# Performance work log

Hardware: AMD Instinct MI355X
Metric: run time of the kernel (lower is better)

The kernel has to match this reference:

```python
import jax, jax.numpy as jnp
import numpy as np

N = 50000      # num nodes
E = 600000     # num edges
D = 128        # num_node_features (in == out)
R = 8          # num_relations


def setup_inputs() -> dict:
    key = jax.random.key(0)
    k = jax.random.split(key, 6)
    x = jax.random.normal(k[0], (N, D), dtype=jnp.float32)
    edge_index = jax.random.randint(k[1], (2, E), 0, N, dtype=jnp.int32)
    edge_type = jax.random.randint(k[2], (E,), 0, R, dtype=jnp.int32)
    scale = 1.0 / np.sqrt(D).astype(np.float32)
    weight = jax.random.normal(k[3], (R, D, D), dtype=jnp.float32) * scale  # per-relation W_r
    root = jax.random.normal(k[4], (D, D), dtype=jnp.float32) * scale       # self-loop weight
    bias = jnp.zeros((D,), dtype=jnp.float32)
    return {"x": x, "edge_index": edge_index, "edge_type": edge_type,
            "weight": weight, "root": root, "bias": bias}


def _rgcn(x, weight, root, bias, edge_index, edge_type):
    # RGCNConv (PyG defaults: aggr='mean' per relation, root weight + bias)
    src, dst = edge_index[0], edge_index[1]
    # combined segment id over (relation, dst) so one segment_sum covers all relations
    seg = edge_type * N + dst                              # [E]
    msgs = x[src]                                          # [E, D] gather
    sums = jax.ops.segment_sum(msgs, seg, num_segments=R * N)                 # [R*N, D]
    cnts = jax.ops.segment_sum(jnp.ones((E, 1), x.dtype), seg, num_segments=R * N)
    mean = sums / jnp.maximum(cnts, 1.0)                   # mean over neighbors, 0 if none
    agg = mean.reshape(R, N, D)
    out = jnp.einsum('rnd,rde->ne', agg, weight) + x @ root + bias
    return out


def reference(x, edge_index, edge_type, weight, root, bias):
    return jax.nn.relu(_rgcn(x, weight, root, bias, edge_index, edge_type))
```

## Files before the change

kernel.cpp:

```cpp
#include <hip/hip_runtime.h>

constexpr int NN = 50000;
constexpr int NE = 600000;
constexpr int D  = 128;
constexpr int NR = 8;
constexpr int KT = (NR + 1) * D;
constexpr int NSEG = NN * NR;

constexpr int SCAN_ELEMS = 1024;
constexpr int NBLK2 = (NSEG + SCAN_ELEMS - 1) / SCAN_ELEMS;

typedef unsigned int   u32;
typedef unsigned short u16;
typedef float  f32x4 __attribute__((ext_vector_type(4)));
typedef short  s16x8 __attribute__((ext_vector_type(8)));

__device__ __forceinline__ u16 f2bf(float f) {
    u32 u = __float_as_uint(f);
    u32 r = (u + 0x7fffu + ((u >> 16) & 1u)) >> 16;
    return (u16)r;
}

__device__ __forceinline__ void async_cp16(const void* g, void* l) {
    __builtin_amdgcn_global_load_lds(
        (const __attribute__((address_space(1))) u32*)g,
        (__attribute__((address_space(3))) u32*)l, 16, 0, 0);
}

__global__ __launch_bounds__(256) void prep_all(const float* __restrict__ x,
                                                const float* __restrict__ weight,
                                                const float* __restrict__ root,
                                                const int* __restrict__ dst,
                                                const int* __restrict__ et,
                                                u16* __restrict__ xb,
                                                u16* __restrict__ wt9,
                                                int* __restrict__ cnt2) {
    const int NX4 = NN * D / 4;
    const int NW  = (NR + 1) * D * D;
    int gid = blockIdx.x * 256 + threadIdx.x;
    if (gid < NX4) {
        int i = gid * 4;
        float4 v = *(const float4*)(x + i);
        ushort4 o;
        o.x = f2bf(v.x); o.y = f2bf(v.y); o.z = f2bf(v.z); o.w = f2bf(v.w);
        *(ushort4*)(xb + i) = o;
        return;
    }
    int g = gid - NX4;
    if (g < NW) {
        int p = g >> 14;
        int idx = g & 16383;
        int n = idx >> 7, k = idx & 127;
        float v = (p == 0) ? root[k * D + n]
                           : weight[(size_t)(p - 1) * D * D + k * D + n];
        wt9[(size_t)p * 16384 + idx] = f2bf(v);
        return;
    }
    int e = g - NW;
    if (e < NE) atomicAdd(&cnt2[dst[e] * NR + et[e]], 1);
}

__global__ __launch_bounds__(256) void scan1(const int* __restrict__ cnt,
                                             int* __restrict__ offs,
                                             int* __restrict__ bsums) {
    __shared__ int lds[256];
    int t = threadIdx.x;
    int base = blockIdx.x * SCAN_ELEMS + t * 4;
    int v0 = (base + 0 < NSEG) ? cnt[base + 0] : 0;
    int v1 = (base + 1 < NSEG) ? cnt[base + 1] : 0;
    int v2 = (base + 2 < NSEG) ? cnt[base + 2] : 0;
    int v3 = (base + 3 < NSEG) ? cnt[base + 3] : 0;
    int s = v0 + v1 + v2 + v3;
    lds[t] = s;
    __syncthreads();
    int val = s;
    for (int off = 1; off < 256; off <<= 1) {
        int tmp = (t >= off) ? lds[t - off] : 0;
        __syncthreads();
        val += tmp;
        lds[t] = val;
        __syncthreads();
    }
    int ex = val - s;
    if (base + 0 < NSEG) offs[base + 0] = ex;
    if (base + 1 < NSEG) offs[base + 1] = ex + v0;
    if (base + 2 < NSEG) offs[base + 2] = ex + v0 + v1;
    if (base + 3 < NSEG) offs[base + 3] = ex + v0 + v1 + v2;
    if (t == 255) bsums[blockIdx.x] = val;
}

__global__ __launch_bounds__(512) void scan2(int* __restrict__ bsums) {
    __shared__ int lds[512];
    int t = threadIdx.x;
    int v = (t < NBLK2) ? bsums[t] : 0;
    lds[t] = v;
    __syncthreads();
    int val = v;
    for (int off = 1; off < 512; off <<= 1) {
        int tmp = (t >= off) ? lds[t - off] : 0;
        __syncthreads();
        val += tmp;
        lds[t] = val;
        __syncthreads();
    }
    if (t < NBLK2) bsums[t] = val - v;
}

__global__ __launch_bounds__(256) void scan3(int* __restrict__ offs,
                                             int* __restrict__ cur,
                                             const int* __restrict__ bsums) {
    int i = blockIdx.x * 256 + threadIdx.x;
    if (i < NSEG) {
        int v = offs[i] + bsums[i >> 10];
        offs[i] = v;
        cur[i]  = v;
    }
    if (i == 0) offs[NSEG] = NE;
}

__global__ __launch_bounds__(256) void fill_bins(const int* __restrict__ src,
                                                 const int* __restrict__ dst,
                                                 const int* __restrict__ et,
                                                 int* __restrict__ cur,
                                                 int* __restrict__ ebin) {
    int e = blockIdx.x * 256 + threadIdx.x;
    if (e >= NE) return;
    int r = et[e];
    int idx = atomicAdd(&cur[dst[e] * NR + r], 1);
    ebin[idx] = (r << 16) | src[e];
}

__global__ __launch_bounds__(128) void aggregate_kernel(const u32* __restrict__ xw,
                                                        const int* __restrict__ offs2,
                                                        const int* __restrict__ ebin,
                                                        u32* __restrict__ sw) {
    const int lane = threadIdx.x & 63;
    const int n = blockIdx.x * 2 + (threadIdx.x >> 6);
    if (n >= NN) return;
    const int beg = __builtin_amdgcn_readfirstlane(offs2[n * NR]);
    const int c   = __builtin_amdgcn_readfirstlane(offs2[n * NR + NR]) - beg;

    float a0 = 0.f, a1 = 0.f;
    int r_cur = 0, cnt_cur = 0;

    int q0 = 0, q1 = 0, q2 = 0, q3 = 0, q4 = 0, q5 = 0, q6 = 0, q7 = 0;
    u32 v0 = 0, v1 = 0, v2 = 0, v3 = 0, v4 = 0, v5 = 0, v6 = 0, v7 = 0;

#define REFILL(Q, V, IDX)                                                   \
    if ((IDX) < c) {                                                        \
        Q = __builtin_amdgcn_readfirstlane(ebin[beg + (IDX)]);              \
        V = xw[(size_t)((u32)Q & 0xffffu) * 64 + lane];                     \
    }
#define FLUSH()                                                             \
    {                                                                       \
        float inv_ = 1.0f / (float)(cnt_cur > 0 ? cnt_cur : 1);             \
        u32 lo16_ = f2bf(a0 * inv_);                                        \
        u32 hi16_ = f2bf(a1 * inv_);                                        \
        sw[((size_t)r_cur * NN + n) * 64 + lane] = lo16_ | (hi16_ << 16);   \
        a0 = 0.f; a1 = 0.f; cnt_cur = 0; ++r_cur;                           \
    }
#define CONSUME(Q, V)                                                       \
    {                                                                       \
        int rj_ = (int)((u32)(Q) >> 16);                                    \
        while (r_cur < rj_) FLUSH()                                         \
        a0 += __uint_as_float((V) << 16);                                   \
        a1 += __uint_as_float((V) & 0xffff0000u);                           \
        ++cnt_cur;                                                          \
    }

    REFILL(q0, v0, 0) REFILL(q1, v1, 1) REFILL(q2, v2, 2) REFILL(q3, v3, 3)
    REFILL(q4, v4, 4) REFILL(q5, v5, 5) REFILL(q6, v6, 6) REFILL(q7, v7, 7)

    int e = 0;
    for (; e + 8 <= c; e += 8) {
        CONSUME(q0, v0) REFILL(q0, v0, e + 8)
        CONSUME(q1, v1) REFILL(q1, v1, e + 9)
        CONSUME(q2, v2) REFILL(q2, v2, e + 10)
        CONSUME(q3, v3) REFILL(q3, v3, e + 11)
        CONSUME(q4, v4) REFILL(q4, v4, e + 12)
        CONSUME(q5, v5) REFILL(q5, v5, e + 13)
        CONSUME(q6, v6) REFILL(q6, v6, e + 14)
        CONSUME(q7, v7) REFILL(q7, v7, e + 15)
    }
    if (e + 0 < c) CONSUME(q0, v0)
    if (e + 1 < c) CONSUME(q1, v1)
    if (e + 2 < c) CONSUME(q2, v2)
    if (e + 3 < c) CONSUME(q3, v3)
    if (e + 4 < c) CONSUME(q4, v4)
    if (e + 5 < c) CONSUME(q5, v5)
    if (e + 6 < c) CONSUME(q6, v6)
    if (e + 7 < c) CONSUME(q7, v7)

    while (r_cur < NR) FLUSH()
#undef REFILL
#undef FLUSH
#undef CONSUME
}

__global__ __launch_bounds__(256) void mfma_gemm(const u16* __restrict__ xb,
                                                 const u16* __restrict__ sums,
                                                 const u16* __restrict__ wt9,
                                                 const float* __restrict__ bias,
                                                 float* __restrict__ out) {
    __shared__ __align__(16) u16 Bs[2][128 * 64];

    const int tid  = threadIdx.x;
    const int wave = tid >> 6;
    const int lane = tid & 63;
    const int m0   = blockIdx.x * 64;
    const int fr   = lane & 15;
    const int l4   = lane >> 4;
    const int fk   = l4 * 8;

    int boff[4];
#pragma unroll
    for (int r = 0; r < 4; ++r) {
        int p = r * 256 + tid;
        int g = p ^ ((p >> 3) & 7);
        boff[r] = (g >> 3) * D + (g & 7) * 8;
    }
    int bidx[16];
#pragma unroll
    for (int h = 0; h < 2; ++h)
#pragma unroll
        for (int nt = 0; nt < 8; ++nt) {
            int gl = (nt * 16 + fr) * 8 + h * 4 + l4;
            int pp = gl ^ ((gl >> 3) & 7);
            bidx[h * 8 + nt] = pp * 8;
        }

    int r0 = m0 + wave * 16 + fr;  if (r0 > NN - 1) r0 = NN - 1;
    const size_t aoff = (size_t)r0 * D + fk;

    auto stage = [&](u16* bufp, const u16* Bp) {
#pragma unroll
        for (int r = 0; r < 4; ++r)
            async_cp16(Bp + boff[r], (char*)bufp + (size_t)(r * 256 + tid) * 16);
    };

    f32x4 acc[8];
#pragma unroll
    for (int j = 0; j < 8; ++j) acc[j] = (f32x4){0.f, 0.f, 0.f, 0.f};

    stage(&Bs[0][0], wt9);
    s16x8 a0c = *(const s16x8*)(xb + aoff);
    s16x8 a1c = *(const s16x8*)(xb + aoff + 32);
    __builtin_amdgcn_sched_barrier(0);

    for (int it = 0; it < 17; ++it) {
        const int nx  = it + 1;
        const int npl = nx >> 1;
        const int kof = (nx & 1) * 64;
        u16* nbuf = &Bs[nx & 1][0];
        const u16* cbuf = &Bs[it & 1][0];

        stage(nbuf, wt9 + npl * 16384 + kof);
        const u16* Ap = ((npl == 0) ? xb : sums + (size_t)(npl - 1) * NN * D) + kof;
        s16x8 a0n = *(const s16x8*)(Ap + aoff);
        s16x8 a1n = *(const s16x8*)(Ap + aoff + 32);
        __builtin_amdgcn_sched_barrier(0);
        asm volatile("s_waitcnt vmcnt(6)" ::: "memory");
        __builtin_amdgcn_s_barrier();
        __builtin_amdgcn_sched_barrier(0);
#pragma unroll
        for (int nt = 0; nt < 8; ++nt) {
            s16x8 bf = *(const s16x8*)(cbuf + bidx[nt]);
            acc[nt] = __builtin_amdgcn_mfma_f32_16x16x32_bf16(a0c, bf, acc[nt], 0, 0, 0);
        }
#pragma unroll
        for (int nt = 0; nt < 8; ++nt) {
            s16x8 bf = *(const s16x8*)(cbuf + bidx[8 + nt]);
            acc[nt] = __builtin_amdgcn_mfma_f32_16x16x32_bf16(a1c, bf, acc[nt], 0, 0, 0);
        }
        asm volatile("s_waitcnt lgkmcnt(0)" ::: "memory");
        __builtin_amdgcn_sched_barrier(0);
        __builtin_amdgcn_s_barrier();
        __builtin_amdgcn_sched_barrier(0);
        a0c = a0n; a1c = a1n;
    }
    asm volatile("s_waitcnt vmcnt(0)" ::: "memory");
    __builtin_amdgcn_s_barrier();
    __builtin_amdgcn_sched_barrier(0);
    {
        const u16* cbuf = &Bs[1][0];
#pragma unroll
        for (int nt = 0; nt < 8; ++nt) {
            s16x8 bf = *(const s16x8*)(cbuf + bidx[nt]);
            acc[nt] = __builtin_amdgcn_mfma_f32_16x16x32_bf16(a0c, bf, acc[nt], 0, 0, 0);
        }
#pragma unroll
        for (int nt = 0; nt < 8; ++nt) {
            s16x8 bf = *(const s16x8*)(cbuf + bidx[8 + nt]);
            acc[nt] = __builtin_amdgcn_mfma_f32_16x16x32_bf16(a1c, bf, acc[nt], 0, 0, 0);
        }
    }

    const int cl = lane & 15;
    const int rq = l4 * 4;
#pragma unroll
    for (int nt = 0; nt < 8; ++nt) {
        int col = nt * 16 + cl;
        float bv = bias[col];
#pragma unroll
        for (int reg = 0; reg < 4; ++reg) {
            int n = m0 + wave * 16 + rq + reg;
            if (n < NN) {
                float v = acc[nt][reg] + bv;
                out[(size_t)n * D + col] = fmaxf(v, 0.0f);
            }
        }
    }
}

extern "C" void kernel_launch(void* const* d_in, const int* in_sizes, int n_in,
                              void* d_out, int out_size, void* d_ws, size_t ws_size,
                              hipStream_t stream) {
    const float* x      = (const float*)d_in[0];
    const int*   ei     = (const int*)d_in[1];
    const int*   et     = (const int*)d_in[2];
    const float* weight = (const float*)d_in[3];
    const float* root   = (const float*)d_in[4];
    const float* bias   = (const float*)d_in[5];
    float* out = (float*)d_out;
    const int* srcv = ei;
    const int* dstv = ei + NE;

    int* cnt2  = (int*)d_ws;
    int* cur2  = cnt2 + NSEG;
    int* offs2 = cur2 + NSEG;
    int* bsums = offs2 + NSEG + 1;
    int* ebin  = bsums + 512;
    size_t fixed_b  = ((char*)(ebin + NE) - (char*)d_ws);
    size_t fixed_al = (fixed_b + 255) & ~(size_t)255;
    u16* xb   = (u16*)((char*)d_ws + fixed_al);
    u16* sums = xb + (size_t)NN * D;
    u16* wt9  = sums + (size_t)NR * NN * D;

    hipMemsetAsync(cnt2, 0, NSEG * sizeof(int), stream);

    const int PREP = NN * D / 4 + (NR + 1) * D * D + NE;
    prep_all<<<(PREP + 255) / 256, 256, 0, stream>>>(x, weight, root, dstv, et,
                                                     xb, wt9, cnt2);

    scan1<<<NBLK2, 256, 0, stream>>>(cnt2, offs2, bsums);
    scan2<<<1, 512, 0, stream>>>(bsums);
    scan3<<<(NSEG + 256) / 256, 256, 0, stream>>>(offs2, cur2, bsums);
    fill_bins<<<(NE + 255) / 256, 256, 0, stream>>>(srcv, dstv, et, cur2, ebin);

    aggregate_kernel<<<(NN + 1) / 2, 128, 0, stream>>>((const u32*)xb, offs2, ebin,
                                                       (u32*)sums);

    mfma_gemm<<<(NN + 63) / 64, 256, 0, stream>>>(xb, sums, wt9, bias, out);
}
```

Baseline: 219.3 us.

## Fuse neighbor aggregation into MFMA GEMM via per-wave LDS scratch

Segments are re-keyed relation-major (rel*N+dst) so each wave can gather the neighbor means for its 16 rows one relation at a time. The means go into a swizzled LDS scratch and feed the MFMA A operand directly, removing the separate aggregate kernel and the 8xNxD bf16 sums buffer round-trip through global memory. The cost is that gather latency now sits inside the GEMM block's schedule. The gather also runs serially per relation with barriers between stages, which may reduce overlap and occupancy because of the extra LDS.

```diff
diff --git a/kernel.cpp b/kernel.cpp
--- a/kernel.cpp
+++ b/kernel.cpp
@@ -4,7 +4,6 @@
 constexpr int NE = 600000;
 constexpr int D  = 128;
 constexpr int NR = 8;
-constexpr int KT = (NR + 1) * D;
 constexpr int NSEG = NN * NR;
 
 constexpr int SCAN_ELEMS = 1024;
@@ -57,7 +56,7 @@
         return;
     }
     int e = g - NW;
-    if (e < NE) atomicAdd(&cnt2[dst[e] * NR + et[e]], 1);
+    if (e < NE) atomicAdd(&cnt2[et[e] * NN + dst[e]], 1);
 }
 
 __global__ __launch_bounds__(256) void scan1(const int* __restrict__ cnt,
@@ -125,92 +124,29 @@
                                                  int* __restrict__ ebin) {
     int e = blockIdx.x * 256 + threadIdx.x;
     if (e >= NE) return;
-    int r = et[e];
-    int idx = atomicAdd(&cur[dst[e] * NR + r], 1);
-    ebin[idx] = (r << 16) | src[e];
-}
-
-__global__ __launch_bounds__(128) void aggregate_kernel(const u32* __restrict__ xw,
-                                                        const int* __restrict__ offs2,
-                                                        const int* __restrict__ ebin,
-                                                        u32* __restrict__ sw) {
-    const int lane = threadIdx.x & 63;
-    const int n = blockIdx.x * 2 + (threadIdx.x >> 6);
-    if (n >= NN) return;
-    const int beg = __builtin_amdgcn_readfirstlane(offs2[n * NR]);
-    const int c   = __builtin_amdgcn_readfirstlane(offs2[n * NR + NR]) - beg;
-
-    float a0 = 0.f, a1 = 0.f;
-    int r_cur = 0, cnt_cur = 0;
-
-    int q0 = 0, q1 = 0, q2 = 0, q3 = 0, q4 = 0, q5 = 0, q6 = 0, q7 = 0;
-    u32 v0 = 0, v1 = 0, v2 = 0, v3 = 0, v4 = 0, v5 = 0, v6 = 0, v7 = 0;
-
-#define REFILL(Q, V, IDX)                                                   \
-    if ((IDX) < c) {                                                        \
-        Q = __builtin_amdgcn_readfirstlane(ebin[beg + (IDX)]);              \
-        V = xw[(size_t)((u32)Q & 0xffffu) * 64 + lane];                     \
-    }
-#define FLUSH()                                                             \
-    {                                                                       \
-        float inv_ = 1.0f / (float)(cnt_cur > 0 ? cnt_cur : 1);             \
-        u32 lo16_ = f2bf(a0 * inv_);                                        \
-        u32 hi16_ = f2bf(a1 * inv_);                                        \
-        sw[((size_t)r_cur * NN + n) * 64 + lane] = lo16_ | (hi16_ << 16);   \
-        a0 = 0.f; a1 = 0.f; cnt_cur = 0; ++r_cur;                           \
-    }
-#define CONSUME(Q, V)                                                       \
-    {                                                                       \
-        int rj_ = (int)((u32)(Q) >> 16);                                    \
-        while (r_cur < rj_) FLUSH()                                         \
-        a0 += __uint_as_float((V) << 16);                                   \
-        a1 += __uint_as_float((V) & 0xffff0000u);                           \
-        ++cnt_cur;                                                          \
-    }
-
-    REFILL(q0, v0, 0) REFILL(q1, v1, 1) REFILL(q2, v2, 2) REFILL(q3, v3, 3)
-    REFILL(q4, v4, 4) REFILL(q5, v5, 5) REFILL(q6, v6, 6) REFILL(q7, v7, 7)
-
-    int e = 0;
-    for (; e + 8 <= c; e += 8) {
-        CONSUME(q0, v0) REFILL(q0, v0, e + 8)
-        CONSUME(q1, v1) REFILL(q1, v1, e + 9)
-        CONSUME(q2, v2) REFILL(q2, v2, e + 10)
-        CONSUME(q3, v3) REFILL(q3, v3, e + 11)
-        CONSUME(q4, v4) REFILL(q4, v4, e + 12)
-        CONSUME(q5, v5) REFILL(q5, v5, e + 13)
-        CONSUME(q6, v6) REFILL(q6, v6, e + 14)
-        CONSUME(q7, v7) REFILL(q7, v7, e + 15)
-    }
-    if (e + 0 < c) CONSUME(q0, v0)
-    if (e + 1 < c) CONSUME(q1, v1)
-    if (e + 2 < c) CONSUME(q2, v2)
-    if (e + 3 < c) CONSUME(q3, v3)
-    if (e + 4 < c) CONSUME(q4, v4)
-    if (e + 5 < c) CONSUME(q5, v5)
-    if (e + 6 < c) CONSUME(q6, v6)
-    if (e + 7 < c) CONSUME(q7, v7)
-
-    while (r_cur < NR) FLUSH()
-#undef REFILL
-#undef FLUSH
-#undef CONSUME
-}
-
-__global__ __launch_bounds__(256) void mfma_gemm(const u16* __restrict__ xb,
-                                                 const u16* __restrict__ sums,
-                                                 const u16* __restrict__ wt9,
-                                                 const float* __restrict__ bias,
-                                                 float* __restrict__ out) {
+    int d = dst[e];
+    int idx = atomicAdd(&cur[et[e] * NN + d], 1);
+    ebin[idx] = (d << 16) | src[e];
+}
+
+__global__ __launch_bounds__(256) void rgcn_fused(const u16* __restrict__ xb,
+                                                  const u16* __restrict__ wt9,
+                                                  const int* __restrict__ offs2,
+                                                  const int* __restrict__ ebin,
+                                                  const float* __restrict__ bias,
+                                                  float* __restrict__ out) {
     __shared__ __align__(16) u16 Bs[2][128 * 64];
+    __shared__ __align__(16) u16 Sc[4][2048];
 
     const int tid  = threadIdx.x;
     const int wave = tid >> 6;
     const int lane = tid & 63;
     const int m0   = blockIdx.x * 64;
+    const int n0   = m0 + wave * 16;
     const int fr   = lane & 15;
     const int l4   = lane >> 4;
-    const int fk   = l4 * 8;
+    const u32* xw  = (const u32*)xb;
+    u16* scratch   = &Sc[wave][0];
 
     int boff[4];
 #pragma unroll
@@ -229,8 +165,10 @@
             bidx[h * 8 + nt] = pp * 8;
         }
 
-    int r0 = m0 + wave * 16 + fr;  if (r0 > NN - 1) r0 = NN - 1;
-    const size_t aoff = (size_t)r0 * D + fk;
+    int sro[4];
+#pragma unroll
+    for (int ks = 0; ks < 4; ++ks)
+        sro[ks] = fr * 128 + (((ks * 4 + l4) ^ (fr & 7)) * 8);
 
     auto stage = [&](u16* bufp, const u16* Bp) {
 #pragma unroll
@@ -238,62 +176,139 @@
             async_cp16(Bp + boff[r], (char*)bufp + (size_t)(r * 256 + tid) * 16);
     };
 
+    auto gather = [&](int rel) {
+        int nlo  = n0 < NN ? n0 : NN;
+        int nhi2 = (n0 + 16) < NN ? (n0 + 16) : NN;
+        int gbeg = __builtin_amdgcn_readfirstlane(offs2[rel * NN + nlo]);
+        int gc   = __builtin_amdgcn_readfirstlane(offs2[rel * NN + nhi2]) - gbeg;
+        float a0 = 0.f, a1 = 0.f;
+        int cur = 0, cnt_cur = 0;
+        int q0 = 0, q1 = 0, q2 = 0, q3 = 0, q4 = 0, q5 = 0, q6 = 0, q7 = 0;
+        u32 w0 = 0, w1 = 0, w2 = 0, w3 = 0, w4 = 0, w5 = 0, w6 = 0, w7 = 0;
+#define GREFILL(Q, V, IDX)                                                  \
+        if ((IDX) < gc) {                                                   \
+            Q = __builtin_amdgcn_readfirstlane(ebin[gbeg + (IDX)]);         \
+            V = xw[(size_t)((u32)Q & 0xffffu) * 64 + lane];                 \
+        }
+#define GFLUSH()                                                            \
+        {                                                                   \
+            float inv_ = 1.0f / (float)(cnt_cur > 0 ? cnt_cur : 1);         \
+            u32 lo_ = f2bf(a0 * inv_);                                      \
+            u32 hi_ = f2bf(a1 * inv_);                                      \
+            *(u32*)(scratch + cur * 128 + (((lane >> 2) ^ (cur & 7)) << 3)  \
+                    + ((2 * lane) & 7)) = lo_ | (hi_ << 16);                \
+            a0 = 0.f; a1 = 0.f; cnt_cur = 0; ++cur;                         \
+        }
+#define GCONSUME(Q, V)                                                      \
+        {                                                                   \
+            int nd_ = (int)((u32)(Q) >> 16) - n0;                           \
+            while (cur < nd_) GFLUSH()                                      \
+            a0 += __uint_as_float((V) << 16);                               \
+            a1 += __uint_as_float((V) & 0xffff0000u);                       \
+            ++cnt_cur;                                                      \
+        }
+        GREFILL(q0, w0, 0) GREFILL(q1, w1, 1) GREFILL(q2, w2, 2) GREFILL(q3, w3, 3)
+        GREFILL(q4, w4, 4) GREFILL(q5, w5, 5) GREFILL(q6, w6, 6) GREFILL(q7, w7, 7)
+        int e = 0;
+        for (; e + 8 <= gc; e += 8) {
+            GCONSUME(q0, w0) GREFILL(q0, w0, e + 8)
+            GCONSUME(q1, w1) GREFILL(q1, w1, e + 9)
+            GCONSUME(q2, w2) GREFILL(q2, w2, e + 10)
+            GCONSUME(q3, w3) GREFILL(q3, w3, e + 11)
+            GCONSUME(q4, w4) GREFILL(q4, w4, e + 12)
+            GCONSUME(q5, w5) GREFILL(q5, w5, e + 13)
+            GCONSUME(q6, w6) GREFILL(q6, w6, e + 14)
+            GCONSUME(q7, w7) GREFILL(q7, w7, e + 15)
+        }
+        if (e + 0 < gc) GCONSUME(q0, w0)
+        if (e + 1 < gc) GCONSUME(q1, w1)
+        if (e + 2 < gc) GCONSUME(q2, w2)
+        if (e + 3 < gc) GCONSUME(q3, w3)
+        if (e + 4 < gc) GCONSUME(q4, w4)
+        if (e + 5 < gc) GCONSUME(q5, w5)
+        if (e + 6 < gc) GCONSUME(q6, w6)
+        if (e + 7 < gc) GCONSUME(q7, w7)
+        while (cur < 16) GFLUSH()
+#undef GREFILL
+#undef GFLUSH
+#undef GCONSUME
+    };
+
+#define FENCE() __builtin_amdgcn_sched_barrier(0)
+#define WAITV4() asm volatile("s_waitcnt vmcnt(4)" ::: "memory")
+#define WAITV0() asm volatile("s_waitcnt vmcnt(0)" ::: "memory")
+#define WAITL0() asm volatile("s_waitcnt lgkmcnt(0)" ::: "memory")
+#define BAR() __builtin_amdgcn_s_barrier()
+#define MFMA8(FA, HB, CB)                                                   \
+    _Pragma("unroll")                                                       \
+    for (int nt = 0; nt < 8; ++nt) {                                        \
+        s16x8 bf = *(const s16x8*)((CB) + bidx[(HB) * 8 + nt]);             \
+        acc[nt] = __builtin_amdgcn_mfma_f32_16x16x32_bf16(FA, bf, acc[nt], 0, 0, 0); \
+    }
+
     f32x4 acc[8];
 #pragma unroll
     for (int j = 0; j < 8; ++j) acc[j] = (f32x4){0.f, 0.f, 0.f, 0.f};
+    s16x8 fa0, fa1, fa2, fa3;
 
     stage(&Bs[0][0], wt9);
-    s16x8 a0c = *(const s16x8*)(xb + aoff);
-    s16x8 a1c = *(const s16x8*)(xb + aoff + 32);
-    __builtin_amdgcn_sched_barrier(0);
-
-    for (int it = 0; it < 17; ++it) {
-        const int nx  = it + 1;
-        const int npl = nx >> 1;
-        const int kof = (nx & 1) * 64;
-        u16* nbuf = &Bs[nx & 1][0];
-        const u16* cbuf = &Bs[it & 1][0];
-
-        stage(nbuf, wt9 + npl * 16384 + kof);
-        const u16* Ap = ((npl == 0) ? xb : sums + (size_t)(npl - 1) * NN * D) + kof;
-        s16x8 a0n = *(const s16x8*)(Ap + aoff);
-        s16x8 a1n = *(const s16x8*)(Ap + aoff + 32);
-        __builtin_amdgcn_sched_barrier(0);
-        asm volatile("s_waitcnt vmcnt(6)" ::: "memory");
-        __builtin_amdgcn_s_barrier();
-        __builtin_amdgcn_sched_barrier(0);
-#pragma unroll
-        for (int nt = 0; nt < 8; ++nt) {
-            s16x8 bf = *(const s16x8*)(cbuf + bidx[nt]);
-            acc[nt] = __builtin_amdgcn_mfma_f32_16x16x32_bf16(a0c, bf, acc[nt], 0, 0, 0);
-        }
-#pragma unroll
-        for (int nt = 0; nt < 8; ++nt) {
-            s16x8 bf = *(const s16x8*)(cbuf + bidx[8 + nt]);
-            acc[nt] = __builtin_amdgcn_mfma_f32_16x16x32_bf16(a1c, bf, acc[nt], 0, 0, 0);
-        }
-        asm volatile("s_waitcnt lgkmcnt(0)" ::: "memory");
-        __builtin_amdgcn_sched_barrier(0);
-        __builtin_amdgcn_s_barrier();
-        __builtin_amdgcn_sched_barrier(0);
-        a0c = a0n; a1c = a1n;
-    }
-    asm volatile("s_waitcnt vmcnt(0)" ::: "memory");
-    __builtin_amdgcn_s_barrier();
-    __builtin_amdgcn_sched_barrier(0);
     {
-        const u16* cbuf = &Bs[1][0];
-#pragma unroll
-        for (int nt = 0; nt < 8; ++nt) {
-            s16x8 bf = *(const s16x8*)(cbuf + bidx[nt]);
-            acc[nt] = __builtin_amdgcn_mfma_f32_16x16x32_bf16(a0c, bf, acc[nt], 0, 0, 0);
-        }
-#pragma unroll
-        for (int nt = 0; nt < 8; ++nt) {
-            s16x8 bf = *(const s16x8*)(cbuf + bidx[8 + nt]);
-            acc[nt] = __builtin_amdgcn_mfma_f32_16x16x32_bf16(a1c, bf, acc[nt], 0, 0, 0);
-        }
-    }
+        int rA = n0 + fr; if (rA > NN - 1) rA = NN - 1;
+        const u16* ap = xb + (size_t)rA * D + l4 * 8;
+        fa0 = *(const s16x8*)(ap);
+        fa1 = *(const s16x8*)(ap + 32);
+        fa2 = *(const s16x8*)(ap + 64);
+        fa3 = *(const s16x8*)(ap + 96);
+    }
+    FENCE();
+
+    gather(0);
+    FENCE();
+    stage(&Bs[1][0], wt9 + 0 * 16384 + 64);
+    FENCE(); WAITV4(); BAR(); FENCE();
+    MFMA8(fa0, 0, &Bs[0][0]) MFMA8(fa1, 1, &Bs[0][0])
+    WAITL0(); FENCE(); BAR(); FENCE();
+    stage(&Bs[0][0], wt9 + 1 * 16384);
+    FENCE(); WAITV4(); BAR(); FENCE();
+    MFMA8(fa2, 0, &Bs[1][0]) MFMA8(fa3, 1, &Bs[1][0])
+    WAITL0(); FENCE(); BAR(); FENCE();
+
+    for (int pl = 1; pl < 8; ++pl) {
+        fa0 = *(const s16x8*)(scratch + sro[0]);
+        fa1 = *(const s16x8*)(scratch + sro[1]);
+        fa2 = *(const s16x8*)(scratch + sro[2]);
+        fa3 = *(const s16x8*)(scratch + sro[3]);
+        WAITL0(); FENCE();
+        gather(pl);
+        FENCE();
+        stage(&Bs[1][0], wt9 + (size_t)pl * 16384 + 64);
+        FENCE(); WAITV4(); BAR(); FENCE();
+        MFMA8(fa0, 0, &Bs[0][0]) MFMA8(fa1, 1, &Bs[0][0])
+        WAITL0(); FENCE(); BAR(); FENCE();
+        stage(&Bs[0][0], wt9 + (size_t)(pl + 1) * 16384);
+        FENCE(); WAITV4(); BAR(); FENCE();
+        MFMA8(fa2, 0, &Bs[1][0]) MFMA8(fa3, 1, &Bs[1][0])
+        WAITL0(); FENCE(); BAR(); FENCE();
+    }
+
+    fa0 = *(const s16x8*)(scratch + sro[0]);
+    fa1 = *(const s16x8*)(scratch + sro[1]);
+    fa2 = *(const s16x8*)(scratch + sro[2]);
+    fa3 = *(const s16x8*)(scratch + sro[3]);
+    WAITL0(); FENCE();
+    stage(&Bs[1][0], wt9 + (size_t)8 * 16384 + 64);
+    FENCE(); WAITV4(); BAR(); FENCE();
+    MFMA8(fa0, 0, &Bs[0][0]) MFMA8(fa1, 1, &Bs[0][0])
+    WAITL0(); FENCE(); BAR(); FENCE();
+    WAITV0(); BAR(); FENCE();
+    MFMA8(fa2, 0, &Bs[1][0]) MFMA8(fa3, 1, &Bs[1][0])
+
+#undef FENCE
+#undef WAITV4
+#undef WAITV0
+#undef WAITL0
+#undef BAR
+#undef MFMA8
 
     const int cl = lane & 15;
     const int rq = l4 * 4;
@@ -333,8 +348,7 @@
     size_t fixed_b  = ((char*)(ebin + NE) - (char*)d_ws);
     size_t fixed_al = (fixed_b + 255) & ~(size_t)255;
     u16* xb   = (u16*)((char*)d_ws + fixed_al);
-    u16* sums = xb + (size_t)NN * D;
-    u16* wt9  = sums + (size_t)NR * NN * D;
+    u16* wt9  = xb + (size_t)NN * D;
 
     hipMemsetAsync(cnt2, 0, NSEG * sizeof(int), stream);
 
@@ -347,8 +361,5 @@
     scan3<<<(NSEG + 256) / 256, 256, 0, stream>>>(offs2, cur2, bsums);
     fill_bins<<<(NE + 255) / 256, 256, 0, stream>>>(srcv, dstv, et, cur2, ebin);
 
-    aggregate_kernel<<<(NN + 1) / 2, 128, 0, stream>>>((const u32*)xb, offs2, ebin,
-                                                       (u32*)sums);
-
-    mfma_gemm<<<(NN + 63) / 64, 256, 0, stream>>>(xb, sums, wt9, bias, out);
-}
+    rgcn_fused<<<(NN + 63) / 64, 256, 0, stream>>>(xb, wt9, offs2, ebin, bias, out);
+}
```

Result: slower. 261.9 us (+19.4%).
